# Kernel tuning notes

Hardware: AMD Instinct MI355X
Metric: run time of the kernel (lower is better)

## Reference

```python
import jax, jax.numpy as jnp
import numpy as np

N = 50000      # nodes
E = 800000     # directed edges
P = 200000     # edge pairs to score
IN_DIM = 32
HID = 64       # per-head hidden dim
HEADS = 4
D = HID * HEADS  # 256, concat output dim
NEG_SLOPE = 0.2  # PyG GATConv leaky_relu slope


def setup_inputs() -> dict:
    key = jax.random.key(0)
    ks = jax.random.split(key, 12)
    return {
        "x": jax.random.normal(ks[0], (N, IN_DIM), jnp.float32),
        "edge_index": jax.random.randint(ks[1], (2, E), 0, N),
        "edge_pairs": jax.random.randint(ks[2], (P, 2), 0, N),
        "W1": jax.random.normal(ks[3], (IN_DIM, D), jnp.float32) / np.float32(np.sqrt(IN_DIM)),
        "att_src1": jax.random.normal(ks[4], (HEADS, HID), jnp.float32) * 0.1,
        "att_dst1": jax.random.normal(ks[5], (HEADS, HID), jnp.float32) * 0.1,
        "b1": jnp.zeros((D,), jnp.float32),
        "W2": jax.random.normal(ks[6], (D, D), jnp.float32) / np.float32(np.sqrt(D)),
        "att_src2": jax.random.normal(ks[7], (HEADS, HID), jnp.float32) * 0.1,
        "att_dst2": jax.random.normal(ks[8], (HEADS, HID), jnp.float32) * 0.1,
        "b2": jnp.zeros((D,), jnp.float32),
        "head_w": jax.random.normal(ks[9], (2 * D, 1), jnp.float32) / np.float32(np.sqrt(2 * D)),
        "head_b": jnp.zeros((1,), jnp.float32),
    }


def _gat_layer(x, src, dst, W, a_src, a_dst, b):
    """PyG-style GATConv (concat=True, self-loops already appended to src/dst)."""
    n = x.shape[0]
    h = (x @ W).reshape(n, HEADS, HID)            # [N,H,C]
    alpha_s = (h * a_src).sum(-1)                  # [N,H]
    alpha_d = (h * a_dst).sum(-1)                  # [N,H]
    e = jax.nn.leaky_relu(alpha_s[src] + alpha_d[dst], NEG_SLOPE)  # [E',H]
    # segment softmax over edges grouped by destination node
    m = jax.ops.segment_max(e, dst, num_segments=n)                # [N,H]
    ex = jnp.exp(e - m[dst])
    denom = jax.ops.segment_sum(ex, dst, num_segments=n)           # [N,H]
    alpha = ex / (denom[dst] + 1e-16)                              # [E',H]
    msg = h[src] * alpha[..., None]                                # [E',H,C]
    out = jax.ops.segment_sum(msg, dst, num_segments=n)            # [N,H,C]
    return out.reshape(n, D) + b


def reference(x, edge_index, edge_pairs, W1, att_src1, att_dst1, b1,
              W2, att_src2, att_dst2, b2, head_w, head_b):
    n = x.shape[0]
    loops = jnp.arange(n, dtype=edge_index.dtype)  # add_self_loops (PyG default)
    src = jnp.concatenate([edge_index[0], loops])
    dst = jnp.concatenate([edge_index[1], loops])
    h = jax.nn.relu(_gat_layer(x, src, dst, W1, att_src1, att_dst1, b1))
    h = jax.nn.relu(_gat_layer(h, src, dst, W2, att_src2, att_dst2, b2))
    pair = jnp.concatenate([h[edge_pairs[:, 0]], h[edge_pairs[:, 1]]], axis=1)  # [P,2D]
    return (pair @ head_w + head_b).squeeze(-1)  # [P]
```

## Files before the change

kernel.cpp:

```cpp
#include <hip/hip_runtime.h>

#define N_NODES 50000
#define E_EDGES 800000
#define E_TOT   (E_EDGES + N_NODES)
#define P_PAIRS 200000
#define IN_DIM  32
#define HID     64
#define HEADS   4
#define D       256
#define NEG_SLOPE 0.2f
#define SCAN_BS 1024
#define LOG2E 1.4426950408889634f

typedef float    f32x4 __attribute__((ext_vector_type(4)));
typedef _Float16 h16x8 __attribute__((ext_vector_type(8)));
typedef _Float16 h16x4 __attribute__((ext_vector_type(4)));

__device__ __forceinline__ float ex2(float v) { return __builtin_amdgcn_exp2f(v); }

__device__ __forceinline__ void edge_sd(const int* __restrict__ ei, int e, int& s, int& d) {
  if (e < E_EDGES) { s = ei[e]; d = ei[E_EDGES + e]; }
  else             { s = d = e - E_EDGES; }
}

__global__ void count_k(const int* __restrict__ ei, int* __restrict__ deg,
                        int* __restrict__ rank) {
  int e = blockIdx.x * 256 + threadIdx.x;
  if (e >= E_TOT) return;
  int s, d; edge_sd(ei, e, s, d);
  rank[e] = atomicAdd(&deg[d], 1);
}

__global__ __launch_bounds__(SCAN_BS) void scan_block_k(const int* __restrict__ in,
                                                        int* __restrict__ out,
                                                        int* __restrict__ bsum, int n) {
  __shared__ int tmp[SCAN_BS];
  int g = blockIdx.x * SCAN_BS + threadIdx.x;
  tmp[threadIdx.x] = (g < n) ? in[g] : 0;
  __syncthreads();
  for (int off = 1; off < SCAN_BS; off <<= 1) {
    int t = 0;
    if ((int)threadIdx.x >= off) t = tmp[threadIdx.x - off];
    __syncthreads();
    if ((int)threadIdx.x >= off) tmp[threadIdx.x] += t;
    __syncthreads();
  }
  if (g < n) out[g] = tmp[threadIdx.x];
  if (threadIdx.x == SCAN_BS - 1) bsum[blockIdx.x] = tmp[SCAN_BS - 1];
}

__global__ void scan_top_k(int* __restrict__ bsum, int nb) {
  __shared__ int tmp[256];
  tmp[threadIdx.x] = ((int)threadIdx.x < nb) ? bsum[threadIdx.x] : 0;
  __syncthreads();
  for (int off = 1; off < 256; off <<= 1) {
    int t = 0;
    if ((int)threadIdx.x >= off) t = tmp[threadIdx.x - off];
    __syncthreads();
    if ((int)threadIdx.x >= off) tmp[threadIdx.x] += t;
    __syncthreads();
  }
  if ((int)threadIdx.x < nb) bsum[threadIdx.x] = tmp[threadIdx.x];
}

__global__ void add_off_k(const int* __restrict__ scan_out,
                          const int* __restrict__ bsum,
                          int* __restrict__ rowptr) {
  int g = blockIdx.x * 256 + threadIdx.x;
  if (g >= N_NODES) return;
  int blk = g / SCAN_BS;
  int add = blk ? bsum[blk - 1] : 0;
  rowptr[g + 1] = scan_out[g] + add;
  if (g == 0) rowptr[0] = 0;
}

__global__ void scatter_k(const int* __restrict__ ei,
                          const int* __restrict__ rowptr,
                          const int* __restrict__ rank, int* __restrict__ csr) {
  int e = blockIdx.x * 256 + threadIdx.x;
  if (e >= E_TOT) return;
  int s, d; edge_sd(ei, e, s, d);
  csr[rowptr[d] + rank[e]] = s;
}

__global__ void prep_k(const float* __restrict__ W1,
                       const float* __restrict__ as1,
                       const float* __restrict__ ad1,
                       const float* __restrict__ W2,
                       float* __restrict__ wa_s, float* __restrict__ wa_d,
                       _Float16* __restrict__ Wt) {
  int g = blockIdx.x * 256 + threadIdx.x;
  int col = g >> 8, k = g & 255;
  Wt[g] = (_Float16)W2[(size_t)k * D + col];
  if (blockIdx.x == 0) {
    int t = threadIdx.x;
    int kk = (t >> 2) & 31, h = t & 3;
    const float* att = (t < 128) ? as1 : ad1;
    float sum = 0.f;
    for (int c = 0; c < HID; ++c) sum += W1[kk * D + h * HID + c] * att[h * HID + c];
    float* dst = (t < 128) ? wa_s : wa_d;
    dst[kk * 4 + h] = sum * LOG2E;
  }
}

__global__ __launch_bounds__(256) void alphas1_k(const float* __restrict__ x,
                                                 const float* __restrict__ wa_s,
                                                 const float* __restrict__ wa_d,
                                                 float* __restrict__ alps,
                                                 float* __restrict__ alpd) {
  int w = (blockIdx.x * 256 + threadIdx.x) >> 6;
  int lane = threadIdx.x & 63;
  int n = w * 8 + (lane >> 3);
  int j = lane & 7;
  float4 xv = make_float4(0.f, 0.f, 0.f, 0.f);
  if (n < N_NODES) xv = *(const float4*)(x + (size_t)n * IN_DIM + j * 4);
  float ps[4] = {0.f, 0.f, 0.f, 0.f}, pd[4] = {0.f, 0.f, 0.f, 0.f};
  #pragma unroll
  for (int kk = 0; kk < 4; ++kk) {
    float xk = ((const float*)&xv)[kk];
    float4 ws = *(const float4*)(wa_s + (j * 4 + kk) * 4);
    float4 wd = *(const float4*)(wa_d + (j * 4 + kk) * 4);
    ps[0] += xk * ws.x; ps[1] += xk * ws.y; ps[2] += xk * ws.z; ps[3] += xk * ws.w;
    pd[0] += xk * wd.x; pd[1] += xk * wd.y; pd[2] += xk * wd.z; pd[3] += xk * wd.w;
  }
  #pragma unroll
  for (int off = 1; off < 8; off <<= 1) {
    #pragma unroll
    for (int h = 0; h < 4; ++h) {
      ps[h] += __shfl_xor(ps[h], off);
      pd[h] += __shfl_xor(pd[h], off);
    }
  }
  if (j == 0 && n < N_NODES) {
    *(float4*)(alps + n * 4) = make_float4(ps[0], ps[1], ps[2], ps[3]);
    *(float4*)(alpd + n * 4) = make_float4(pd[0], pd[1], pd[2], pd[3]);
  }
}

__global__ __launch_bounds__(256) void gat_gather1_k(
    const int* __restrict__ rowptr, const int* __restrict__ csr,
    const float* __restrict__ alps, const float* __restrict__ alpd,
    const float* __restrict__ x, float* __restrict__ agg) {
  int wid2 = (blockIdx.x * 256 + threadIdx.x) >> 6;
  int lane = threadIdx.x & 63;
  int half = lane >> 5, l = lane & 31;
  int n = wid2 * 2 + half;
  bool valid = n < N_NODES;
  int q = l >> 3;
  int kk = (l & 7) * 4;
  int beg = valid ? rowptr[n] : 0;
  int end = valid ? rowptr[n + 1] : 0;
  float ad = valid ? alpd[n * HEADS + q] : 0.f;

  float den = 0.f;
  float4 acc = make_float4(0.f, 0.f, 0.f, 0.f);

  for (int i = beg; i < end; i += 8) {
    int s[8]; bool ok[8]; float xl[8]; float4 xv[8];
    #pragma unroll
    for (int j = 0; j < 8; ++j) { ok[j] = (i + j) < end; s[j] = ok[j] ? csr[i + j] : 0; }
    #pragma unroll
    for (int j = 0; j < 8; ++j) xl[j] = alps[s[j] * HEADS + q];
    #pragma unroll
    for (int j = 0; j < 8; ++j) xv[j] = *(const float4*)(x + (size_t)s[j] * IN_DIM + kk);
    float e[8];
    #pragma unroll
    for (int j = 0; j < 8; ++j) {
      float t = xl[j] + ad;
      t = fmaxf(t, NEG_SLOPE * t);
      e[j] = ok[j] ? ex2(t) : 0.f;
    }
    den += (((e[0] + e[1]) + (e[2] + e[3])) + ((e[4] + e[5]) + (e[6] + e[7])));
    #pragma unroll
    for (int j = 0; j < 8; ++j) {
      acc.x = fmaf(e[j], xv[j].x, acc.x);
      acc.y = fmaf(e[j], xv[j].y, acc.y);
      acc.z = fmaf(e[j], xv[j].z, acc.z);
      acc.w = fmaf(e[j], xv[j].w, acc.w);
    }
  }
  if (valid) {
    float inv = 1.f / (den + 1e-16f);
    float4 o = make_float4(acc.x * inv, acc.y * inv, acc.z * inv, acc.w * inv);
    *(float4*)(agg + (size_t)n * 128 + l * 4) = o;
  }
}

__global__ __launch_bounds__(256) void gemm_head1(const float* __restrict__ agg,
                                                  const float* __restrict__ W,
                                                  const float* __restrict__ b,
                                                  _Float16* __restrict__ A16) {
  __shared__ float As[32][68];
  __shared__ float Bs[32][64];
  const int row0 = blockIdx.x * 64;
  const int q = blockIdx.y;
  const int col0 = q * 64;
  const int t = threadIdx.x, tx = t & 15, ty = t >> 4;
  #pragma unroll
  for (int i = 0; i < 2; ++i) {
    int idx = t + i * 256;
    int r = idx >> 3, k4 = idx & 7;
    int rr = row0 + r;
    float4 a = make_float4(0.f, 0.f, 0.f, 0.f);
    if (rr < N_NODES) a = *(const float4*)(agg + (size_t)rr * 128 + q * 32 + k4 * 4);
    As[k4 * 4 + 0][r] = a.x;
    As[k4 * 4 + 1][r] = a.y;
    As[k4 * 4 + 2][r] = a.z;
    As[k4 * 4 + 3][r] = a.w;
  }
  #pragma unroll
  for (int i = 0; i < 2; ++i) {
    int idx = t + i * 256;
    int k = idx >> 4, c4 = idx & 15;
    *(float4*)&Bs[k][c4 * 4] = *(const float4*)(W + (size_t)k * D + col0 + c4 * 4);
  }
  __syncthreads();
  float acc[4][4] = {{0.f}};
  #pragma unroll
  for (int k = 0; k < 32; ++k) {
    float4 av = *(const float4*)&As[k][ty * 4];
    float4 bv = *(const float4*)&Bs[k][tx * 4];
    acc[0][0] += av.x * bv.x; acc[0][1] += av.x * bv.y;
    acc[0][2] += av.x * bv.z; acc[0][3] += av.x * bv.w;
    acc[1][0] += av.y * bv.x; acc[1][1] += av.y * bv.y;
    acc[1][2] += av.y * bv.z; acc[1][3] += av.y * bv.w;
    acc[2][0] += av.z * bv.x; acc[2][1] += av.z * bv.y;
    acc[2][2] += av.z * bv.z; acc[2][3] += av.z * bv.w;
    acc[3][0] += av.w * bv.x; acc[3][1] += av.w * bv.y;
    acc[3][2] += av.w * bv.z; acc[3][3] += av.w * bv.w;
  }
  float4 bv = *(const float4*)(b + col0 + tx * 4);
  const float bb[4] = {bv.x, bv.y, bv.z, bv.w};
  #pragma unroll
  for (int i = 0; i < 4; ++i) {
    int rr = row0 + ty * 4 + i;
    if (rr < N_NODES) {
      h16x4 o4;
      #pragma unroll
      for (int j = 0; j < 4; ++j)
        o4[j] = (_Float16)fmaxf(acc[i][j] + bb[j], 0.f);
      *(h16x4*)(A16 + (size_t)rr * D + col0 + tx * 4) = o4;
    }
  }
}

__global__ __launch_bounds__(256) void gemm2_mfma(
    const _Float16* __restrict__ A16, const _Float16* __restrict__ Wt,
    const float* __restrict__ asrc, const float* __restrict__ adst,
    _Float16* __restrict__ h2, float* __restrict__ alps, float* __restrict__ alpd) {
  __shared__ __attribute__((aligned(16))) _Float16 As[128][40];
  __shared__ __attribute__((aligned(16))) _Float16 Bs[128][40];
  const int row0 = blockIdx.x * 128;
  const int col0 = blockIdx.y * 128;
  const int t = threadIdx.x;
  const int wave = t >> 6, lane = t & 63;
  const int wr = wave >> 1, wc = wave & 1;
  const int lg = lane >> 4, li = lane & 15;

  f32x4 acc[4][4];
  #pragma unroll
  for (int m = 0; m < 4; ++m)
    #pragma unroll
    for (int n = 0; n < 4; ++n) acc[m][n] = (f32x4)0.f;

  for (int kc = 0; kc < D; kc += 32) {
    #pragma unroll
    for (int i = 0; i < 2; ++i) {
      int idx = t + i * 256;
      int r = idx >> 2, seg = idx & 3;
      int rr = row0 + r;
      uint4 va = make_uint4(0, 0, 0, 0);
      if (rr < N_NODES) va = *(const uint4*)(A16 + (size_t)rr * D + kc + seg * 8);
      *(uint4*)&As[r][seg * 8] = va;
      uint4 vb = *(const uint4*)(Wt + (size_t)(col0 + r) * D + kc + seg * 8);
      *(uint4*)&Bs[r][seg * 8] = vb;
    }
    __syncthreads();
    h16x8 af[4], bf[4];
    #pragma unroll
    for (int m = 0; m < 4; ++m)
      af[m] = *(const h16x8*)&As[wr * 64 + m * 16 + li][lg * 8];
    #pragma unroll
    for (int n = 0; n < 4; ++n)
      bf[n] = *(const h16x8*)&Bs[wc * 64 + n * 16 + li][lg * 8];
    #pragma unroll
    for (int m = 0; m < 4; ++m)
      #pragma unroll
      for (int n = 0; n < 4; ++n)
        acc[m][n] = __builtin_amdgcn_mfma_f32_16x16x32_f16(af[m], bf[n], acc[m][n], 0, 0, 0);
    __syncthreads();
  }

  #pragma unroll
  for (int m = 0; m < 4; ++m) {
    #pragma unroll
    for (int reg = 0; reg < 4; ++reg) {
      int rr = row0 + wr * 64 + m * 16 + lg * 4 + reg;
      if (rr < N_NODES) {
        #pragma unroll
        for (int n = 0; n < 4; ++n)
          h2[(size_t)rr * D + col0 + wc * 64 + n * 16 + li] = (_Float16)acc[m][n][reg];
      }
    }
  }

  const int q = blockIdx.y * 2 + wc;
  float wsv[4], wdv[4];
  #pragma unroll
  for (int n = 0; n < 4; ++n) {
    wsv[n] = asrc[q * HID + n * 16 + li];
    wdv[n] = adst[q * HID + n * 16 + li];
  }
  #pragma unroll
  for (int m = 0; m < 4; ++m) {
    #pragma unroll
    for (int reg = 0; reg < 4; ++reg) {
      float ps = acc[m][0][reg] * wsv[0] + acc[m][1][reg] * wsv[1]
               + acc[m][2][reg] * wsv[2] + acc[m][3][reg] * wsv[3];
      float pd = acc[m][0][reg] * wdv[0] + acc[m][1][reg] * wdv[1]
               + acc[m][2][reg] * wdv[2] + acc[m][3][reg] * wdv[3];
      #pragma unroll
      for (int off = 1; off < 16; off <<= 1) {
        ps += __shfl_xor(ps, off);
        pd += __shfl_xor(pd, off);
      }
      int rr = row0 + wr * 64 + m * 16 + lg * 4 + reg;
      if (li == 0 && rr < N_NODES) {
        alps[rr * HEADS + q] = ps * LOG2E;
        alpd[rr * HEADS + q] = pd * LOG2E;
      }
    }
  }
}

__global__ __launch_bounds__(256) void gat_gather2_k(
    const int* __restrict__ rowptr, const int* __restrict__ csr,
    const float* __restrict__ alps, const float* __restrict__ alpd,
    const _Float16* __restrict__ h, const float* __restrict__ b,
    const float* __restrict__ hw,
    float* __restrict__ u, float* __restrict__ v) {
  int wid2 = (blockIdx.x * 256 + threadIdx.x) >> 6;
  int lane = threadIdx.x & 63;
  int half = lane >> 5, l = lane & 31;
  int n = wid2 * 2 + half;
  bool valid = n < N_NODES;
  int q = l >> 3;
  int beg = valid ? rowptr[n] : 0;
  int end = valid ? rowptr[n + 1] : 0;
  float ad = valid ? alpd[n * HEADS + q] : 0.f;

  float den = 0.f;
  float acc[8] = {0.f, 0.f, 0.f, 0.f, 0.f, 0.f, 0.f, 0.f};

  for (int i = beg; i < end; i += 8) {
    int s[8]; bool ok[8]; float xl[8]; h16x8 hv[8];
    #pragma unroll
    for (int j = 0; j < 8; ++j) { ok[j] = (i + j) < end; s[j] = ok[j] ? csr[i + j] : 0; }
    #pragma unroll
    for (int j = 0; j < 8; ++j) xl[j] = alps[s[j] * HEADS + q];
    #pragma unroll
    for (int j = 0; j < 8; ++j) hv[j] = *(const h16x8*)(h + (size_t)s[j] * D + l * 8);
    float e[8];
    #pragma unroll
    for (int j = 0; j < 8; ++j) {
      float t = xl[j] + ad;
      t = fmaxf(t, NEG_SLOPE * t);
      e[j] = ok[j] ? ex2(t) : 0.f;
    }
    den += (((e[0] + e[1]) + (e[2] + e[3])) + ((e[4] + e[5]) + (e[6] + e[7])));
    #pragma unroll
    for (int ch = 0; ch < 8; ++ch) {
      float a = acc[ch];
      #pragma unroll
      for (int j = 0; j < 8; ++j)
        a = fmaf((float)hv[j][ch], e[j], a);
      acc[ch] = a;
    }
  }

  float inv = 1.f / (den + 1e-16f);
  float4 b0 = *(const float4*)(b + l * 8);
  float4 b1 = *(const float4*)(b + l * 8 + 4);
  float4 w00 = *(const float4*)(hw + l * 8);
  float4 w01 = *(const float4*)(hw + l * 8 + 4);
  float4 w10 = *(const float4*)(hw + D + l * 8);
  float4 w11 = *(const float4*)(hw + D + l * 8 + 4);
  const float* bb[2] = {(const float*)&b0, (const float*)&b1};
  const float* w0p[2] = {(const float*)&w00, (const float*)&w01};
  const float* w1p[2] = {(const float*)&w10, (const float*)&w11};
  float su = 0.f, sv = 0.f;
  #pragma unroll
  for (int ch = 0; ch < 8; ++ch) {
    float o = fmaxf(acc[ch] * inv + bb[ch >> 2][ch & 3], 0.f);
    su = fmaf(o, w0p[ch >> 2][ch & 3], su);
    sv = fmaf(o, w1p[ch >> 2][ch & 3], sv);
  }
  #pragma unroll
  for (int off = 16; off; off >>= 1) {
    su += __shfl_xor(su, off);
    sv += __shfl_xor(sv, off);
  }
  if (l == 0 && valid) { u[n] = su; v[n] = sv; }
}

__global__ void pair_lu_k(const int* __restrict__ pairs,
                          const float* __restrict__ u, const float* __restrict__ v,
                          const float* __restrict__ hb, float* __restrict__ out) {
  int g = blockIdx.x * 256 + threadIdx.x;
  if (g >= P_PAIRS) return;
  int a = pairs[g * 2], b = pairs[g * 2 + 1];
  out[g] = u[a] + v[b] + hb[0];
}

extern "C" void kernel_launch(void* const* d_in, const int* in_sizes, int n_in,
                              void* d_out, int out_size, void* d_ws, size_t ws_size,
                              hipStream_t stream) {
  const float* x    = (const float*)d_in[0];
  const int*   ei   = (const int*)d_in[1];
  const int*   prs  = (const int*)d_in[2];
  const float* W1   = (const float*)d_in[3];
  const float* as1  = (const float*)d_in[4];
  const float* ad1  = (const float*)d_in[5];
  const float* b1   = (const float*)d_in[6];
  const float* W2   = (const float*)d_in[7];
  const float* as2  = (const float*)d_in[8];
  const float* ad2  = (const float*)d_in[9];
  const float* b2   = (const float*)d_in[10];
  const float* hw   = (const float*)d_in[11];
  const float* hb   = (const float*)d_in[12];
  float* out = (float*)d_out;

  const int NPAD = 50048;

  char* w = (char*)d_ws;
  float* buf0 = (float*)w;             w += (size_t)N_NODES * D * 4;
  float* alps = (float*)w;             w += (size_t)N_NODES * HEADS * 4;
  float* alpd = (float*)w;             w += (size_t)N_NODES * HEADS * 4;
  int* rowptr = (int*)w;               w += (size_t)(N_NODES + 1) * 4;
  int* csr    = (int*)w;               w += (size_t)E_TOT * 4;
  float* uu   = (float*)w;             w += (size_t)N_NODES * 4;
  float* vv   = (float*)w;             w += (size_t)N_NODES * 4;
  float* wa_s = (float*)w;             w += 128 * 4;
  float* wa_d = (float*)w;             w += 128 * 4;
  _Float16* A16 = (_Float16*)w;        w += (size_t)NPAD * D * 2;
  _Float16* Wt  = (_Float16*)w;        w += (size_t)D * D * 2;

  _Float16* h2f16 = (_Float16*)buf0;

  int* deg      = (int*)buf0;
  int* scan_out = deg + N_NODES;
  int* bsum     = scan_out + N_NODES;
  int* rank     = bsum + 64;

  const int eBlk     = (E_TOT + 255) / 256;
  const int nScanBlk = (N_NODES + SCAN_BS - 1) / SCAN_BS;
  const int nBlk256  = (N_NODES + 255) / 256;
  const int a1Blk    = (N_NODES * 8 + 255) / 256;
  const int g1Blk    = ((N_NODES + 1) / 2 * 64 + 255) / 256;
  const int pairBlk  = (P_PAIRS + 255) / 256;
  const dim3 headGrid((N_NODES + 63) / 64, HEADS);
  const dim3 mfmaGrid(NPAD / 128, D / 128);

  hipMemsetAsync(deg, 0, (size_t)N_NODES * 4, stream);
  count_k<<<eBlk, 256, 0, stream>>>(ei, deg, rank);
  scan_block_k<<<nScanBlk, SCAN_BS, 0, stream>>>(deg, scan_out, bsum, N_NODES);
  scan_top_k<<<1, 256, 0, stream>>>(bsum, nScanBlk);
  add_off_k<<<nBlk256, 256, 0, stream>>>(scan_out, bsum, rowptr);
  scatter_k<<<eBlk, 256, 0, stream>>>(ei, rowptr, rank, csr);

  prep_k<<<D * D / 256, 256, 0, stream>>>(W1, as1, ad1, W2, wa_s, wa_d, Wt);

  alphas1_k<<<a1Blk, 256, 0, stream>>>(x, wa_s, wa_d, alps, alpd);
  gat_gather1_k<<<g1Blk, 256, 0, stream>>>(rowptr, csr, alps, alpd, x, buf0);
  gemm_head1<<<headGrid, 256, 0, stream>>>(buf0, W1, b1, A16);

  gemm2_mfma<<<mfmaGrid, 256, 0, stream>>>(A16, Wt, as2, ad2, h2f16, alps, alpd);
  gat_gather2_k<<<g1Blk, 256, 0, stream>>>(rowptr, csr, alps, alpd, h2f16, b2, hw, uu, vv);

  pair_lu_k<<<pairBlk, 256, 0, stream>>>(prs, uu, vv, hb, out);
}
```

Measured before the change: 320.5 us.

## Merge preprocessing kernels into fewer launches and shrink gather2 unroll to six

Folds the weight-prep work into the degree-count kernel and the alpha1 computation into the CSR scatter kernel using block-index partitioning. The top-level scan kernel is removed by having add_off_k sum the block sums serially (at most 49 per thread). The layer-2 gather loop is unrolled by six instead of eight, presumably to lower register pressure and raise occupancy. The aim is to cut kernel launch count and the idle gaps between launches, in exchange for heterogeneous blocks and a little redundant summation.

New measurement: 311.2 us. 1.03x faster.

```diff
diff --git a/kernel.cpp b/kernel.cpp
--- a/kernel.cpp
+++ b/kernel.cpp
@@ -23,12 +23,33 @@
   else             { s = d = e - E_EDGES; }
 }
 
-__global__ void count_k(const int* __restrict__ ei, int* __restrict__ deg,
-                        int* __restrict__ rank) {
-  int e = blockIdx.x * 256 + threadIdx.x;
-  if (e >= E_TOT) return;
-  int s, d; edge_sd(ei, e, s, d);
-  rank[e] = atomicAdd(&deg[d], 1);
+__global__ void count_prep_k(const int* __restrict__ ei, int* __restrict__ deg,
+                             int* __restrict__ rank,
+                             const float* __restrict__ W1,
+                             const float* __restrict__ as1,
+                             const float* __restrict__ ad1,
+                             const float* __restrict__ W2,
+                             float* __restrict__ wa_s, float* __restrict__ wa_d,
+                             _Float16* __restrict__ Wt) {
+  if (blockIdx.x < 256) {
+    int g = blockIdx.x * 256 + threadIdx.x;
+    int col = g >> 8, k = g & 255;
+    Wt[g] = (_Float16)W2[(size_t)k * D + col];
+    if (blockIdx.x == 0) {
+      int t = threadIdx.x;
+      int kk = (t >> 2) & 31, h = t & 3;
+      const float* att = (t < 128) ? as1 : ad1;
+      float sum = 0.f;
+      for (int c = 0; c < HID; ++c) sum += W1[kk * D + h * HID + c] * att[h * HID + c];
+      float* dst = (t < 128) ? wa_s : wa_d;
+      dst[kk * 4 + h] = sum * LOG2E;
+    }
+  } else {
+    int e = (blockIdx.x - 256) * 256 + threadIdx.x;
+    if (e >= E_TOT) return;
+    int s, d; edge_sd(ei, e, s, d);
+    rank[e] = atomicAdd(&deg[d], 1);
+  }
 }
 
 __global__ __launch_bounds__(SCAN_BS) void scan_block_k(const int* __restrict__ in,
@@ -49,91 +70,57 @@
   if (threadIdx.x == SCAN_BS - 1) bsum[blockIdx.x] = tmp[SCAN_BS - 1];
 }
 
-__global__ void scan_top_k(int* __restrict__ bsum, int nb) {
-  __shared__ int tmp[256];
-  tmp[threadIdx.x] = ((int)threadIdx.x < nb) ? bsum[threadIdx.x] : 0;
-  __syncthreads();
-  for (int off = 1; off < 256; off <<= 1) {
-    int t = 0;
-    if ((int)threadIdx.x >= off) t = tmp[threadIdx.x - off];
-    __syncthreads();
-    if ((int)threadIdx.x >= off) tmp[threadIdx.x] += t;
-    __syncthreads();
-  }
-  if ((int)threadIdx.x < nb) bsum[threadIdx.x] = tmp[threadIdx.x];
-}
-
 __global__ void add_off_k(const int* __restrict__ scan_out,
                           const int* __restrict__ bsum,
                           int* __restrict__ rowptr) {
   int g = blockIdx.x * 256 + threadIdx.x;
   if (g >= N_NODES) return;
   int blk = g / SCAN_BS;
-  int add = blk ? bsum[blk - 1] : 0;
+  int add = 0;
+  for (int b = 0; b < blk; ++b) add += bsum[b];
   rowptr[g + 1] = scan_out[g] + add;
   if (g == 0) rowptr[0] = 0;
 }
 
-__global__ void scatter_k(const int* __restrict__ ei,
-                          const int* __restrict__ rowptr,
-                          const int* __restrict__ rank, int* __restrict__ csr) {
-  int e = blockIdx.x * 256 + threadIdx.x;
-  if (e >= E_TOT) return;
-  int s, d; edge_sd(ei, e, s, d);
-  csr[rowptr[d] + rank[e]] = s;
-}
-
-__global__ void prep_k(const float* __restrict__ W1,
-                       const float* __restrict__ as1,
-                       const float* __restrict__ ad1,
-                       const float* __restrict__ W2,
-                       float* __restrict__ wa_s, float* __restrict__ wa_d,
-                       _Float16* __restrict__ Wt) {
-  int g = blockIdx.x * 256 + threadIdx.x;
-  int col = g >> 8, k = g & 255;
-  Wt[g] = (_Float16)W2[(size_t)k * D + col];
-  if (blockIdx.x == 0) {
-    int t = threadIdx.x;
-    int kk = (t >> 2) & 31, h = t & 3;
-    const float* att = (t < 128) ? as1 : ad1;
-    float sum = 0.f;
-    for (int c = 0; c < HID; ++c) sum += W1[kk * D + h * HID + c] * att[h * HID + c];
-    float* dst = (t < 128) ? wa_s : wa_d;
-    dst[kk * 4 + h] = sum * LOG2E;
-  }
-}
-
-__global__ __launch_bounds__(256) void alphas1_k(const float* __restrict__ x,
-                                                 const float* __restrict__ wa_s,
-                                                 const float* __restrict__ wa_d,
-                                                 float* __restrict__ alps,
-                                                 float* __restrict__ alpd) {
-  int w = (blockIdx.x * 256 + threadIdx.x) >> 6;
-  int lane = threadIdx.x & 63;
-  int n = w * 8 + (lane >> 3);
-  int j = lane & 7;
-  float4 xv = make_float4(0.f, 0.f, 0.f, 0.f);
-  if (n < N_NODES) xv = *(const float4*)(x + (size_t)n * IN_DIM + j * 4);
-  float ps[4] = {0.f, 0.f, 0.f, 0.f}, pd[4] = {0.f, 0.f, 0.f, 0.f};
-  #pragma unroll
-  for (int kk = 0; kk < 4; ++kk) {
-    float xk = ((const float*)&xv)[kk];
-    float4 ws = *(const float4*)(wa_s + (j * 4 + kk) * 4);
-    float4 wd = *(const float4*)(wa_d + (j * 4 + kk) * 4);
-    ps[0] += xk * ws.x; ps[1] += xk * ws.y; ps[2] += xk * ws.z; ps[3] += xk * ws.w;
-    pd[0] += xk * wd.x; pd[1] += xk * wd.y; pd[2] += xk * wd.z; pd[3] += xk * wd.w;
-  }
-  #pragma unroll
-  for (int off = 1; off < 8; off <<= 1) {
-    #pragma unroll
-    for (int h = 0; h < 4; ++h) {
-      ps[h] += __shfl_xor(ps[h], off);
-      pd[h] += __shfl_xor(pd[h], off);
-    }
-  }
-  if (j == 0 && n < N_NODES) {
-    *(float4*)(alps + n * 4) = make_float4(ps[0], ps[1], ps[2], ps[3]);
-    *(float4*)(alpd + n * 4) = make_float4(pd[0], pd[1], pd[2], pd[3]);
+__global__ __launch_bounds__(256) void scatter_alphas_k(
+    const int* __restrict__ ei, const int* __restrict__ rowptr,
+    const int* __restrict__ rank, int* __restrict__ csr,
+    const float* __restrict__ x,
+    const float* __restrict__ wa_s, const float* __restrict__ wa_d,
+    float* __restrict__ alps, float* __restrict__ alpd, int a1Blk) {
+  if ((int)blockIdx.x < a1Blk) {
+    int w = (blockIdx.x * 256 + threadIdx.x) >> 6;
+    int lane = threadIdx.x & 63;
+    int n = w * 8 + (lane >> 3);
+    int j = lane & 7;
+    float4 xv = make_float4(0.f, 0.f, 0.f, 0.f);
+    if (n < N_NODES) xv = *(const float4*)(x + (size_t)n * IN_DIM + j * 4);
+    float ps[4] = {0.f, 0.f, 0.f, 0.f}, pd[4] = {0.f, 0.f, 0.f, 0.f};
+    #pragma unroll
+    for (int kk = 0; kk < 4; ++kk) {
+      float xk = ((const float*)&xv)[kk];
+      float4 ws = *(const float4*)(wa_s + (j * 4 + kk) * 4);
+      float4 wd = *(const float4*)(wa_d + (j * 4 + kk) * 4);
+      ps[0] += xk * ws.x; ps[1] += xk * ws.y; ps[2] += xk * ws.z; ps[3] += xk * ws.w;
+      pd[0] += xk * wd.x; pd[1] += xk * wd.y; pd[2] += xk * wd.z; pd[3] += xk * wd.w;
+    }
+    #pragma unroll
+    for (int off = 1; off < 8; off <<= 1) {
+      #pragma unroll
+      for (int h = 0; h < 4; ++h) {
+        ps[h] += __shfl_xor(ps[h], off);
+        pd[h] += __shfl_xor(pd[h], off);
+      }
+    }
+    if (j == 0 && n < N_NODES) {
+      *(float4*)(alps + n * 4) = make_float4(ps[0], ps[1], ps[2], ps[3]);
+      *(float4*)(alpd + n * 4) = make_float4(pd[0], pd[1], pd[2], pd[3]);
+    }
+  } else {
+    int e = (blockIdx.x - a1Blk) * 256 + threadIdx.x;
+    if (e >= E_TOT) return;
+    int s, d; edge_sd(ei, e, s, d);
+    csr[rowptr[d] + rank[e]] = s;
   }
 }
 
@@ -352,28 +339,31 @@
   float den = 0.f;
   float acc[8] = {0.f, 0.f, 0.f, 0.f, 0.f, 0.f, 0.f, 0.f};
 
-  for (int i = beg; i < end; i += 8) {
-    int s[8]; bool ok[8]; float xl[8]; h16x8 hv[8];
-    #pragma unroll
-    for (int j = 0; j < 8; ++j) { ok[j] = (i + j) < end; s[j] = ok[j] ? csr[i + j] : 0; }
-    #pragma unroll
-    for (int j = 0; j < 8; ++j) xl[j] = alps[s[j] * HEADS + q];
-    #pragma unroll
-    for (int j = 0; j < 8; ++j) hv[j] = *(const h16x8*)(h + (size_t)s[j] * D + l * 8);
-    float e[8];
-    #pragma unroll
-    for (int j = 0; j < 8; ++j) {
+  for (int i = beg; i < end; i += 6) {
+    int s[6]; bool ok[6]; float xl[6]; h16x8 hv[6];
+    #pragma unroll
+    for (int j = 0; j < 6; ++j) { ok[j] = (i + j) < end; s[j] = ok[j] ? csr[i + j] : 0; }
+    #pragma unroll
+    for (int j = 0; j < 6; ++j) xl[j] = alps[s[j] * HEADS + q];
+    #pragma unroll
+    for (int j = 0; j < 6; ++j) hv[j] = *(const h16x8*)(h + (size_t)s[j] * D + l * 8);
+    float e[6];
+    #pragma unroll
+    for (int j = 0; j < 6; ++j) {
       float t = xl[j] + ad;
       t = fmaxf(t, NEG_SLOPE * t);
       e[j] = ok[j] ? ex2(t) : 0.f;
     }
-    den += (((e[0] + e[1]) + (e[2] + e[3])) + ((e[4] + e[5]) + (e[6] + e[7])));
+    den += ((e[0] + e[1]) + (e[2] + e[3])) + (e[4] + e[5]);
     #pragma unroll
     for (int ch = 0; ch < 8; ++ch) {
       float a = acc[ch];
-      #pragma unroll
-      for (int j = 0; j < 8; ++j)
-        a = fmaf((float)hv[j][ch], e[j], a);
+      a = fmaf((float)hv[0][ch], e[0], a);
+      a = fmaf((float)hv[1][ch], e[1], a);
+      a = fmaf((float)hv[2][ch], e[2], a);
+      a = fmaf((float)hv[3][ch], e[3], a);
+      a = fmaf((float)hv[4][ch], e[4], a);
+      a = fmaf((float)hv[5][ch], e[5], a);
       acc[ch] = a;
     }
   }
@@ -462,15 +452,13 @@
   const dim3 mfmaGrid(NPAD / 128, D / 128);
 
   hipMemsetAsync(deg, 0, (size_t)N_NODES * 4, stream);
-  count_k<<<eBlk, 256, 0, stream>>>(ei, deg, rank);
+  count_prep_k<<<256 + eBlk, 256, 0, stream>>>(ei, deg, rank,
+                                               W1, as1, ad1, W2, wa_s, wa_d, Wt);
   scan_block_k<<<nScanBlk, SCAN_BS, 0, stream>>>(deg, scan_out, bsum, N_NODES);
-  scan_top_k<<<1, 256, 0, stream>>>(bsum, nScanBlk);
   add_off_k<<<nBlk256, 256, 0, stream>>>(scan_out, bsum, rowptr);
-  scatter_k<<<eBlk, 256, 0, stream>>>(ei, rowptr, rank, csr);
-
-  prep_k<<<D * D / 256, 256, 0, stream>>>(W1, as1, ad1, W2, wa_s, wa_d, Wt);
-
-  alphas1_k<<<a1Blk, 256, 0, stream>>>(x, wa_s, wa_d, alps, alpd);
+  scatter_alphas_k<<<a1Blk + eBlk, 256, 0, stream>>>(ei, rowptr, rank, csr,
+                                                     x, wa_s, wa_d, alps, alpd, a1Blk);
+
   gat_gather1_k<<<g1Blk, 256, 0, stream>>>(rowptr, csr, alps, alpd, x, buf0);
   gemm_head1<<<headGrid, 256, 0, stream>>>(buf0, W1, b1, A16);
 
```
